# Optimization experiments

Hardware: AMD Instinct MI355X
Metric: run time of the kernel (lower is better)

Reference implementation:

```python
import jax, jax.numpy as jnp
import numpy as np

NUM_HEADS = 16
NUM_KV_HEADS = 4
HEAD_DIM = 128
ROPE_THETA = 10000.0


def _rope_cos_sin(T, dim, theta):
    inv_freq = 1.0 / (theta ** (jnp.arange(0, dim, 2, dtype=jnp.float32) / dim))
    freqs = jnp.arange(T, dtype=jnp.float32)[:, None] * inv_freq[None, :]  # (T, dim/2)
    emb = jnp.concatenate([freqs, freqs], axis=-1)  # (T, dim)
    return jnp.cos(emb), jnp.sin(emb)


def _rotate_half(x):
    h = x.shape[-1] // 2
    return jnp.concatenate([-x[..., h:], x[..., :h]], axis=-1)


def _apply_rope(x, cos, sin):
    # x: (B, H, T, D); cos/sin: (T, D)
    return x * cos[None, None] + _rotate_half(x) * sin[None, None]


def setup_inputs() -> dict:
    key = jax.random.key(0)
    ks = jax.random.split(key, 6)
    B, T, H = 2, 2048, 2048
    latent = 256
    kv_dim = NUM_KV_HEADS * HEAD_DIM
    s = 0.02
    return {
        "x": jax.random.normal(ks[0], (B, T, H), jnp.float32),
        "wq": jax.random.normal(ks[1], (H, H), jnp.float32) * s,
        "wkv": jax.random.normal(ks[2], (latent, H), jnp.float32) * s,
        "wk": jax.random.normal(ks[3], (kv_dim, latent), jnp.float32) * s,
        "wv": jax.random.normal(ks[4], (kv_dim, latent), jnp.float32) * s,
        "wo": jax.random.normal(ks[5], (H, H), jnp.float32) * s,
    }


def reference(x, wq, wkv, wk, wv, wo):
    B, T, hidden = x.shape
    nh, nkv, hd = NUM_HEADS, NUM_KV_HEADS, HEAD_DIM

    q = jnp.einsum('bth,dh->btd', x, wq)
    kv_latent = jnp.einsum('bth,lh->btl', x, wkv)
    k = jnp.einsum('btl,dl->btd', kv_latent, wk)
    v = jnp.einsum('btl,dl->btd', kv_latent, wv)

    q = q.reshape(B, T, nh, hd).transpose(0, 2, 1, 3)   # (B, nh, T, hd)
    k = k.reshape(B, T, nkv, hd).transpose(0, 2, 1, 3)  # (B, nkv, T, hd)
    v = v.reshape(B, T, nkv, hd).transpose(0, 2, 1, 3)

    cos, sin = _rope_cos_sin(T, hd, ROPE_THETA)
    q = _apply_rope(q, cos, sin)
    k = _apply_rope(k, cos, sin)

    rep = nh // nkv
    k = jnp.repeat(k, rep, axis=1)  # (B, nh, T, hd)
    v = jnp.repeat(v, rep, axis=1)

    scores = jnp.einsum('bhqd,bhkd->bhqk', q, k) * (1.0 / np.sqrt(hd))
    causal = jnp.triu(jnp.ones((T, T), dtype=bool), k=1)
    scores = jnp.where(causal[None, None], -jnp.inf, scores)
    probs = jax.nn.softmax(scores, axis=-1)
    out = jnp.einsum('bhqk,bhkd->bhqd', probs, v)
    out = out.transpose(0, 2, 1, 3).reshape(B, T, nh * hd)
    return jnp.einsum('btd,hd->bth', out, wo)
```

## Files before the change

kernel.cpp:

```cpp
#include <hip/hip_runtime.h>
#include <math.h>


#define AS1 __attribute__((address_space(1)))
#define AS3 __attribute__((address_space(3)))
#define QSTRIDE 2304

typedef short bf16x8 __attribute__((ext_vector_type(8)));
typedef float f32x4 __attribute__((ext_vector_type(4)));
typedef float f32x16 __attribute__((ext_vector_type(16)));
typedef unsigned int uint32x2 __attribute__((ext_vector_type(2)));

__device__ __forceinline__ unsigned short f2bf(float x) {
  union { float f; unsigned int u; } q; q.f = x;
  unsigned int u = q.u;
  u += 0x7FFFu + ((u >> 16) & 1u);
  return (unsigned short)(u >> 16);
}
__device__ __forceinline__ float bf2f(unsigned short x) {
  union { unsigned int u; float f; } q; q.u = ((unsigned int)x) << 16;
  return q.f;
}
__device__ __forceinline__ unsigned int pack2bf(float a, float b) {
  return (unsigned int)f2bf(a) | ((unsigned int)f2bf(b) << 16);
}
__device__ __forceinline__ uint32x2 plswap(unsigned int a, unsigned int b) {
  return __builtin_amdgcn_permlane32_swap(a, b, false, false);
}
__device__ __forceinline__ float xor32_add(float x) {
  union { float f; unsigned int u; } X; X.f = x;
  uint32x2 r = plswap(X.u, X.u);
  union { unsigned int u; float f; } A, B; A.u = r.x; B.u = r.y;
  return A.f + B.f;
}

__global__ __launch_bounds__(256) void rope_table(float* __restrict__ cost,
                                                  float* __restrict__ sint,
                                                  int T) {
  int idx = blockIdx.x * 256 + threadIdx.x;
  if (idx >= T * 64) return;
  int t = idx >> 6, j = idx & 63;
  double invf = pow(10000.0, -(double)j / 64.0);
  double ang = (double)t * invf;
  cost[idx] = (float)cos(ang);
  sint[idx] = (float)sin(ang);
}

__global__ __launch_bounds__(256) void conv_bf16(const float* __restrict__ src,
                                                 unsigned short* __restrict__ dst,
                                                 int n) {
  int i = (blockIdx.x * 256 + threadIdx.x) * 4;
  if (i >= n) return;
  float4 f = *(const float4*)(src + i);
  ushort4 o;
  o.x = f2bf(f.x); o.y = f2bf(f.y); o.z = f2bf(f.z); o.w = f2bf(f.w);
  *(ushort4*)(dst + i) = o;
}

template <bool OUT_BF16>
__global__ __launch_bounds__(256) void gemm_mfma(const unsigned short* __restrict__ A,
                                                 const unsigned short* __restrict__ W,
                                                 void* __restrict__ Cv,
                                                 int M, int N, int K,
                                                 int lda, int ldw, int ldc) {
  __shared__ unsigned short Asl[2][128 * 32];
  __shared__ unsigned short Wsl[2][128 * 32];
  int tid = threadIdx.x;
  int w = tid >> 6, lane = tid & 63;
  int g = lane >> 4, c = lane & 15;
  int wm = w >> 1, wn = w & 1;
  int m0 = blockIdx.y * 128, n0 = blockIdx.x * 128;

  f32x4 acc[4][4] = {};

#pragma unroll
  for (int i = 0; i < 2; ++i) {
    int idx = i * 256 + tid;
    int row = idx >> 2;
    int kk = (idx & 3) * 8;
    __builtin_amdgcn_global_load_lds(
        (const AS1 void*)(A + (size_t)(m0 + row) * lda + kk),
        (AS3 void*)(Asl[0] + ((size_t)i * 256 + (w << 6)) * 8), 16, 0, 0);
    __builtin_amdgcn_global_load_lds(
        (const AS1 void*)(W + (size_t)(n0 + row) * ldw + kk),
        (AS3 void*)(Wsl[0] + ((size_t)i * 256 + (w << 6)) * 8), 16, 0, 0);
  }
  __syncthreads();

  int cur = 0;
  for (int k0 = 0; k0 < K; k0 += 32) {
    if (k0 + 32 < K) {
      int nb = cur ^ 1;
#pragma unroll
      for (int i = 0; i < 2; ++i) {
        int idx = i * 256 + tid;
        int row = idx >> 2;
        int kk = (idx & 3) * 8;
        __builtin_amdgcn_global_load_lds(
            (const AS1 void*)(A + (size_t)(m0 + row) * lda + k0 + 32 + kk),
            (AS3 void*)(Asl[nb] + ((size_t)i * 256 + (w << 6)) * 8), 16, 0, 0);
        __builtin_amdgcn_global_load_lds(
            (const AS1 void*)(W + (size_t)(n0 + row) * ldw + k0 + 32 + kk),
            (AS3 void*)(Wsl[nb] + ((size_t)i * 256 + (w << 6)) * 8), 16, 0, 0);
      }
    }
    bf16x8 af[4], wf[4];
#pragma unroll
    for (int mi = 0; mi < 4; ++mi)
      af[mi] = *(const bf16x8*)(Asl[cur] + (wm * 64 + mi * 16 + c) * 32 + g * 8);
#pragma unroll
    for (int ni = 0; ni < 4; ++ni)
      wf[ni] = *(const bf16x8*)(Wsl[cur] + (wn * 64 + ni * 16 + c) * 32 + g * 8);
#pragma unroll
    for (int mi = 0; mi < 4; ++mi)
#pragma unroll
      for (int ni = 0; ni < 4; ++ni)
        acc[mi][ni] = __builtin_amdgcn_mfma_f32_16x16x32_bf16(af[mi], wf[ni],
                                                              acc[mi][ni], 0, 0, 0);
    __syncthreads();
    cur ^= 1;
  }
#pragma unroll
  for (int mi = 0; mi < 4; ++mi)
#pragma unroll
    for (int r = 0; r < 4; ++r) {
      size_t mrow = (size_t)(m0 + wm * 64 + mi * 16 + g * 4 + r) * ldc;
#pragma unroll
      for (int ni = 0; ni < 4; ++ni) {
        int n = n0 + wn * 64 + ni * 16 + c;
        if (OUT_BF16)
          ((unsigned short*)Cv)[mrow + n] = f2bf(acc[mi][ni][r]);
        else
          ((float*)Cv)[mrow + n] = acc[mi][ni][r];
      }
    }
}

__global__ __launch_bounds__(256) void rope_ip_bf16(unsigned short* __restrict__ buf,
                                                    int nheads, int T, int rowstride,
                                                    const float* __restrict__ cost,
                                                    const float* __restrict__ sint,
                                                    float scale) {
  int idx = blockIdx.x * 256 + threadIdx.x;
  int d = idx & 63;
  int rest = idx >> 6;
  int h = rest % nheads;
  int bt = rest / nheads;
  int t = bt & (T - 1);
  unsigned short* p = buf + (size_t)bt * rowstride + h * 128;
  float cc = cost[t * 64 + d], ss = sint[t * 64 + d];
  float x0 = bf2f(p[d]), x1 = bf2f(p[d + 64]);
  p[d]      = f2bf((x0 * cc - x1 * ss) * scale);
  p[d + 64] = f2bf((x1 * cc + x0 * ss) * scale);
}

__global__ __launch_bounds__(256) void rope_pack_k(const unsigned short* __restrict__ kvcat,
                                                   unsigned short* __restrict__ kp,
                                                   const float* __restrict__ cost,
                                                   const float* __restrict__ sint) {
  int idx = blockIdx.x * 256 + threadIdx.x;
  int d = idx & 63;
  int rest = idx >> 6;
  int kvh = rest & 3;
  int bt = rest >> 2;
  int t = bt & 2047, b = bt >> 11;
  const unsigned short* src = kvcat + (size_t)bt * 1024 + kvh * 128;
  float cc = cost[t * 64 + d], ss = sint[t * 64 + d];
  float x0 = bf2f(src[d]), x1 = bf2f(src[d + 64]);
  unsigned short y0 = f2bf(x0 * cc - x1 * ss);
  unsigned short y1 = f2bf(x1 * cc + x0 * ss);
  int kr = t & 63;
  size_t base = (size_t)(b * 4 + kvh) * 262144 + (size_t)(t >> 6) * 8192;
  kp[base + ((kr * 128 + d)      ^ ((kr & 7) << 3))] = y0;
  kp[base + ((kr * 128 + d + 64) ^ ((kr & 7) << 3))] = y1;
}

__global__ __launch_bounds__(256) void transpose_v(const unsigned short* __restrict__ kvcat,
                                                   unsigned short* __restrict__ vp) {
  __shared__ unsigned short tile[32][33];
  int t0 = blockIdx.x * 32, d0 = blockIdx.y * 32, b = blockIdx.z;
  int tx = threadIdx.x & 31, ty = threadIdx.x >> 5;
#pragma unroll
  for (int i = 0; i < 4; ++i) {
    int t = ty + i * 8;
    tile[t][tx] = kvcat[((size_t)(b * 2048 + t0 + t)) * 1024 + 512 + d0 + tx];
  }
  __syncthreads();
#pragma unroll
  for (int i = 0; i < 4; ++i) {
    int dd = ty + i * 8;
    int D = d0 + dd;
    int d = D & 127;
    int t = t0 + tx;
    size_t base = (size_t)(b * 4 + (D >> 7)) * 262144 + (size_t)(t >> 6) * 8192;
    vp[base + ((d * 64 + (t & 63)) ^ ((d & 7) << 3))] = tile[tx][dd];
  }
}

__global__ __launch_bounds__(256, 2) void attn_mfma(const unsigned short* __restrict__ qb,
                                                    const unsigned short* __restrict__ kp,
                                                    const unsigned short* __restrict__ vp,
                                                    unsigned short* __restrict__ attob) {
  __shared__ unsigned short kimg[2][8192];
  __shared__ unsigned short vimg[2][8192];

  int tid = threadIdx.x;
  int w = tid >> 6, lane = tid & 63;
  int cl = lane & 31, hi = lane >> 5;
  int stream = blockIdx.x & 31;
  int gseq = blockIdx.x >> 5;
  int g = (gseq & 1) ? (15 - (gseq >> 1)) : (gseq >> 1);
  int h = stream & 15, b = stream >> 4;
  int kvh = h >> 2;
  int q0w = g * 128 + w * 32;
  int nt = 2 * g + 2;

  const unsigned short* kpS = kp + (size_t)(b * 4 + kvh) * 262144;
  const unsigned short* vpS = vp + (size_t)(b * 4 + kvh) * 262144;

  bf16x8 qa[8];
  {
    const unsigned short* qrow = qb + ((size_t)(b * 2048 + q0w + cl)) * QSTRIDE + h * 128 + hi * 8;
#pragma unroll
    for (int kc = 0; kc < 8; ++kc)
      qa[kc] = *(const bf16x8*)(qrow + kc * 16);
  }

  f32x16 o0 = {}, o1 = {}, o2 = {}, o3 = {};
  float l = 0.f;

#pragma unroll
  for (int i = 0; i < 4; ++i) {
    __builtin_amdgcn_global_load_lds(
        (const AS1 void*)(kpS + (size_t)w * 2048 + i * 512 + lane * 8),
        (AS3 void*)(&kimg[0][w * 2048 + i * 512]), 16, 0, 0);
    __builtin_amdgcn_global_load_lds(
        (const AS1 void*)(vpS + (size_t)w * 2048 + i * 512 + lane * 8),
        (AS3 void*)(&vimg[0][w * 2048 + i * 512]), 16, 0, 0);
  }
  __syncthreads();

  int cur = 0;
  for (int ti = 0; ti < nt; ++ti) {
    if (ti + 1 < nt) {
      size_t src = (size_t)(ti + 1) * 8192 + w * 2048 + lane * 8;
      int nb = cur ^ 1;
#pragma unroll
      for (int i = 0; i < 4; ++i) {
        __builtin_amdgcn_global_load_lds(
            (const AS1 void*)(kpS + src + i * 512),
            (AS3 void*)(&kimg[nb][w * 2048 + i * 512]), 16, 0, 0);
        __builtin_amdgcn_global_load_lds(
            (const AS1 void*)(vpS + src + i * 512),
            (AS3 void*)(&vimg[nb][w * 2048 + i * 512]), 16, 0, 0);
      }
    }
#pragma unroll
    for (int s = 0; s < 2; ++s) {
      int ks0 = ti * 64 + s * 32;
      if (ks0 > q0w) continue;
      bf16x8 kf[8];
#pragma unroll
      for (int kc = 0; kc < 8; ++kc)
        kf[kc] = *(const bf16x8*)&kimg[cur][((s * 32 + cl) * 128 + kc * 16 + hi * 8)
                                            ^ ((cl & 7) << 3)];
      f32x16 sS = {};
      __builtin_amdgcn_s_setprio(1);
#pragma unroll
      for (int kc = 0; kc < 8; ++kc)
        sS = __builtin_amdgcn_mfma_f32_32x32x16_bf16(kf[kc], qa[kc], sS, 0, 0, 0);
      __builtin_amdgcn_s_setprio(0);
      bf16x8 vf[8];
#pragma unroll
      for (int db = 0; db < 4; ++db)
#pragma unroll
        for (int ks = 0; ks < 2; ++ks)
          vf[db * 2 + ks] = *(const bf16x8*)&vimg[cur][((db * 32 + cl) * 64
                              + s * 32 + ks * 16 + hi * 8) ^ ((cl & 7) << 3)];
      if (ks0 == q0w) {
#pragma unroll
        for (int r = 0; r < 16; ++r) {
          int krow = (r & 3) + 8 * (r >> 2) + 4 * hi;
          if (krow > cl) sS[r] = -INFINITY;
        }
      }
      float p[16];
      float rs = 0.f;
#pragma unroll
      for (int r = 0; r < 16; ++r) { p[r] = __expf(sS[r]); rs += p[r]; }
      l += rs;
      union { unsigned int u[4]; bf16x8 v; } pb0, pb1;
      {
        uint32x2 r0 = plswap(pack2bf(p[0], p[1]), pack2bf(p[4], p[5]));
        uint32x2 r1 = plswap(pack2bf(p[2], p[3]), pack2bf(p[6], p[7]));
        pb0.u[0] = r0.x; pb0.u[1] = r1.x; pb0.u[2] = r0.y; pb0.u[3] = r1.y;
        uint32x2 r2 = plswap(pack2bf(p[8], p[9]), pack2bf(p[12], p[13]));
        uint32x2 r3 = plswap(pack2bf(p[10], p[11]), pack2bf(p[14], p[15]));
        pb1.u[0] = r2.x; pb1.u[1] = r3.x; pb1.u[2] = r2.y; pb1.u[3] = r3.y;
      }
      __builtin_amdgcn_s_setprio(1);
      o0 = __builtin_amdgcn_mfma_f32_32x32x16_bf16(vf[0], pb0.v, o0, 0, 0, 0);
      o1 = __builtin_amdgcn_mfma_f32_32x32x16_bf16(vf[2], pb0.v, o1, 0, 0, 0);
      o2 = __builtin_amdgcn_mfma_f32_32x32x16_bf16(vf[4], pb0.v, o2, 0, 0, 0);
      o3 = __builtin_amdgcn_mfma_f32_32x32x16_bf16(vf[6], pb0.v, o3, 0, 0, 0);
      o0 = __builtin_amdgcn_mfma_f32_32x32x16_bf16(vf[1], pb1.v, o0, 0, 0, 0);
      o1 = __builtin_amdgcn_mfma_f32_32x32x16_bf16(vf[3], pb1.v, o1, 0, 0, 0);
      o2 = __builtin_amdgcn_mfma_f32_32x32x16_bf16(vf[5], pb1.v, o2, 0, 0, 0);
      o3 = __builtin_amdgcn_mfma_f32_32x32x16_bf16(vf[7], pb1.v, o3, 0, 0, 0);
      __builtin_amdgcn_s_setprio(0);
    }
    __syncthreads();
    cur ^= 1;
  }

  float lsum = xor32_add(l);
  float inv = 1.f / lsum;
  int q = q0w + cl;
  unsigned short* obase = attob + ((size_t)(b * 2048 + q)) * 2048 + h * 128;
#pragma unroll
  for (int r = 0; r < 16; ++r) {
    int dl = (r & 3) + 8 * (r >> 2) + 4 * hi;
    obase[dl]      = f2bf(o0[r] * inv);
    obase[32 + dl] = f2bf(o1[r] * inv);
    obase[64 + dl] = f2bf(o2[r] * inv);
    obase[96 + dl] = f2bf(o3[r] * inv);
  }
}

extern "C" void kernel_launch(void* const* d_in, const int* in_sizes, int n_in,
                              void* d_out, int out_size, void* d_ws, size_t ws_size,
                              hipStream_t stream) {
  const float* x   = (const float*)d_in[0];
  const float* wq  = (const float*)d_in[1];
  const float* wkv = (const float*)d_in[2];
  const float* wk  = (const float*)d_in[3];
  const float* wv  = (const float*)d_in[4];
  const float* wo  = (const float*)d_in[5];
  float* out = (float*)d_out;
  float* ws  = (float*)d_ws;

  const int B = 2, T = 2048, H = 2048, NH = 16, NKV = 4, LAT = 256, KVD = 512;
  const int BT = B * T;

  size_t off = 0;
  unsigned short* xb    = (unsigned short*)(ws + off); off += (size_t)BT * H / 2;
  unsigned short* wqb   = (unsigned short*)(ws + off); off += (size_t)H * H / 2;
  unsigned short* wkvb  = (unsigned short*)(ws + off); off += (size_t)LAT * H / 2;
  unsigned short* wkb   = (unsigned short*)(ws + off); off += (size_t)KVD * LAT / 2;
  unsigned short* wvb   = (unsigned short*)(ws + off); off += (size_t)KVD * LAT / 2;
  unsigned short* wob   = (unsigned short*)(ws + off); off += (size_t)H * H / 2;
  unsigned short* qkv   = (unsigned short*)(ws + off); off += (size_t)BT * QSTRIDE / 2;
  unsigned short* kvcat = (unsigned short*)(ws + off); off += (size_t)BT * 1024 / 2;
  unsigned short* kp    = (unsigned short*)(ws + off); off += (size_t)BT * KVD / 2;
  unsigned short* vp    = (unsigned short*)(ws + off); off += (size_t)BT * KVD / 2;
  unsigned short* attob = (unsigned short*)(ws + off); off += (size_t)BT * H / 2;
  float* cost = ws + off; off += (size_t)T * 64;
  float* sint = ws + off; off += (size_t)T * 64;

  const float scale = 0.088388347648318447f;

  rope_table<<<(T * 64 + 255) / 256, 256, 0, stream>>>(cost, sint, T);

  conv_bf16<<<(BT * H / 4) / 256, 256, 0, stream>>>(x, xb, BT * H);
  conv_bf16<<<(H * H / 4) / 256, 256, 0, stream>>>(wq, wqb, H * H);
  conv_bf16<<<(LAT * H / 4) / 256, 256, 0, stream>>>(wkv, wkvb, LAT * H);
  conv_bf16<<<(KVD * LAT / 4) / 256, 256, 0, stream>>>(wk, wkb, KVD * LAT);
  conv_bf16<<<(KVD * LAT / 4) / 256, 256, 0, stream>>>(wv, wvb, KVD * LAT);
  conv_bf16<<<(H * H / 4) / 256, 256, 0, stream>>>(wo, wob, H * H);

  gemm_mfma<true><<<dim3(QSTRIDE / 128, BT / 128), 256, 0, stream>>>(
      xb, wqb, qkv, BT, QSTRIDE, H, H, H, QSTRIDE);
  gemm_mfma<true><<<dim3(1024 / 128, BT / 128), 256, 0, stream>>>(
      qkv + H, wkb, kvcat, BT, 1024, LAT, QSTRIDE, LAT, 1024);

  rope_ip_bf16<<<(BT * NH * 64) / 256, 256, 0, stream>>>(qkv, NH, T, QSTRIDE, cost, sint, scale);
  rope_pack_k<<<(BT * NKV * 64) / 256, 256, 0, stream>>>(kvcat, kp, cost, sint);
  transpose_v<<<dim3(T / 32, KVD / 32, B), 256, 0, stream>>>(kvcat, vp);

  attn_mfma<<<512, 256, 0, stream>>>(qkv, kp, vp, attob);

  gemm_mfma<false><<<dim3(H / 128, BT / 128), 256, 0, stream>>>(
      attob, wob, out, BT, H, H, H, H, H);
}
```

Before: 231.8 us.

## Split attention KV tiles across waves with shared-memory reduction and smaller blocks

The attention kernel now uses 64-query blocks instead of 128, launches twice as many blocks, and uses 32-key tiles instead of 64-key tiles. Pairs of waves split the key tiles between them (even/odd) and combine their partial outputs and row sums through shared memory at the end. The K/V packing kernels change to a 32-row tile layout to match. LDS use per block drops, so the launch bound rises to 4 blocks per SM. This is meant to improve occupancy and load balance on the causal triangle. In exchange it adds a final reduction, rounds the partial outputs to bf16 before summing, and doubles the tile iterations per block.

```diff
diff --git a/kernel.cpp b/kernel.cpp
--- a/kernel.cpp
+++ b/kernel.cpp
@@ -169,8 +169,8 @@
   float x0 = bf2f(src[d]), x1 = bf2f(src[d + 64]);
   unsigned short y0 = f2bf(x0 * cc - x1 * ss);
   unsigned short y1 = f2bf(x1 * cc + x0 * ss);
-  int kr = t & 63;
-  size_t base = (size_t)(b * 4 + kvh) * 262144 + (size_t)(t >> 6) * 8192;
+  int kr = t & 31;
+  size_t base = (size_t)(b * 4 + kvh) * 262144 + (size_t)(t >> 5) * 4096;
   kp[base + ((kr * 128 + d)      ^ ((kr & 7) << 3))] = y0;
   kp[base + ((kr * 128 + d + 64) ^ ((kr & 7) << 3))] = y1;
 }
@@ -192,28 +192,27 @@
     int D = d0 + dd;
     int d = D & 127;
     int t = t0 + tx;
-    size_t base = (size_t)(b * 4 + (D >> 7)) * 262144 + (size_t)(t >> 6) * 8192;
-    vp[base + ((d * 64 + (t & 63)) ^ ((d & 7) << 3))] = tile[tx][dd];
-  }
-}
-
-__global__ __launch_bounds__(256, 2) void attn_mfma(const unsigned short* __restrict__ qb,
+    size_t base = (size_t)(b * 4 + (D >> 7)) * 262144 + (size_t)(t >> 5) * 4096;
+    vp[base + ((d * 32 + (t & 31)) ^ ((d & 3) << 3))] = tile[tx][dd];
+  }
+}
+
+__global__ __launch_bounds__(256, 4) void attn_mfma(const unsigned short* __restrict__ qb,
                                                     const unsigned short* __restrict__ kp,
                                                     const unsigned short* __restrict__ vp,
                                                     unsigned short* __restrict__ attob) {
-  __shared__ unsigned short kimg[2][8192];
-  __shared__ unsigned short vimg[2][8192];
+  __shared__ unsigned short smem[16896];
 
   int tid = threadIdx.x;
   int w = tid >> 6, lane = tid & 63;
+  int wq = w >> 1, wk = w & 1;
   int cl = lane & 31, hi = lane >> 5;
   int stream = blockIdx.x & 31;
-  int gseq = blockIdx.x >> 5;
-  int g = (gseq & 1) ? (15 - (gseq >> 1)) : (gseq >> 1);
+  int G = 31 - (blockIdx.x >> 5);
   int h = stream & 15, b = stream >> 4;
   int kvh = h >> 2;
-  int q0w = g * 128 + w * 32;
-  int nt = 2 * g + 2;
+  int q0w = G * 64 + wq * 32;
+  int nt = 2 * G + 2;
 
   const unsigned short* kpS = kp + (size_t)(b * 4 + kvh) * 262144;
   const unsigned short* vpS = vp + (size_t)(b * 4 + kvh) * 262144;
@@ -230,40 +229,39 @@
   float l = 0.f;
 
 #pragma unroll
-  for (int i = 0; i < 4; ++i) {
+  for (int i = 0; i < 2; ++i) {
     __builtin_amdgcn_global_load_lds(
-        (const AS1 void*)(kpS + (size_t)w * 2048 + i * 512 + lane * 8),
-        (AS3 void*)(&kimg[0][w * 2048 + i * 512]), 16, 0, 0);
+        (const AS1 void*)(kpS + (size_t)w * 1024 + i * 512 + lane * 8),
+        (AS3 void*)(&smem[w * 1024 + i * 512]), 16, 0, 0);
     __builtin_amdgcn_global_load_lds(
-        (const AS1 void*)(vpS + (size_t)w * 2048 + i * 512 + lane * 8),
-        (AS3 void*)(&vimg[0][w * 2048 + i * 512]), 16, 0, 0);
+        (const AS1 void*)(vpS + (size_t)w * 1024 + i * 512 + lane * 8),
+        (AS3 void*)(&smem[8192 + w * 1024 + i * 512]), 16, 0, 0);
   }
   __syncthreads();
 
   int cur = 0;
   for (int ti = 0; ti < nt; ++ti) {
     if (ti + 1 < nt) {
-      size_t src = (size_t)(ti + 1) * 8192 + w * 2048 + lane * 8;
+      size_t src = (size_t)(ti + 1) * 4096 + w * 1024 + lane * 8;
       int nb = cur ^ 1;
 #pragma unroll
-      for (int i = 0; i < 4; ++i) {
+      for (int i = 0; i < 2; ++i) {
         __builtin_amdgcn_global_load_lds(
             (const AS1 void*)(kpS + src + i * 512),
-            (AS3 void*)(&kimg[nb][w * 2048 + i * 512]), 16, 0, 0);
+            (AS3 void*)(&smem[nb * 4096 + w * 1024 + i * 512]), 16, 0, 0);
         __builtin_amdgcn_global_load_lds(
             (const AS1 void*)(vpS + src + i * 512),
-            (AS3 void*)(&vimg[nb][w * 2048 + i * 512]), 16, 0, 0);
+            (AS3 void*)(&smem[8192 + nb * 4096 + w * 1024 + i * 512]), 16, 0, 0);
       }
     }
-#pragma unroll
-    for (int s = 0; s < 2; ++s) {
-      int ks0 = ti * 64 + s * 32;
-      if (ks0 > q0w) continue;
+    int ks0 = ti << 5;
+    if (((ti & 1) == wk) && (ks0 <= q0w)) {
+      const unsigned short* kb_ = &smem[cur * 4096];
+      const unsigned short* vb_ = &smem[8192 + cur * 4096];
       bf16x8 kf[8];
 #pragma unroll
       for (int kc = 0; kc < 8; ++kc)
-        kf[kc] = *(const bf16x8*)&kimg[cur][((s * 32 + cl) * 128 + kc * 16 + hi * 8)
-                                            ^ ((cl & 7) << 3)];
+        kf[kc] = *(const bf16x8*)&kb_[(cl * 128 + kc * 16 + hi * 8) ^ ((cl & 7) << 3)];
       f32x16 sS = {};
       __builtin_amdgcn_s_setprio(1);
 #pragma unroll
@@ -275,8 +273,8 @@
       for (int db = 0; db < 4; ++db)
 #pragma unroll
         for (int ks = 0; ks < 2; ++ks)
-          vf[db * 2 + ks] = *(const bf16x8*)&vimg[cur][((db * 32 + cl) * 64
-                              + s * 32 + ks * 16 + hi * 8) ^ ((cl & 7) << 3)];
+          vf[db * 2 + ks] = *(const bf16x8*)&vb_[((db * 32 + cl) * 32
+                              + ks * 16 + hi * 8) ^ ((cl & 3) << 3)];
       if (ks0 == q0w) {
 #pragma unroll
         for (int r = 0; r < 16; ++r) {
@@ -314,16 +312,37 @@
   }
 
   float lsum = xor32_add(l);
-  float inv = 1.f / lsum;
-  int q = q0w + cl;
-  unsigned short* obase = attob + ((size_t)(b * 2048 + q)) * 2048 + h * 128;
+  float* lptr = (float*)&smem[16384];
+  int qr = wq * 32 + cl;
+  if (hi == 0) lptr[wk * 64 + qr] = lsum;
 #pragma unroll
   for (int r = 0; r < 16; ++r) {
     int dl = (r & 3) + 8 * (r >> 2) + 4 * hi;
-    obase[dl]      = f2bf(o0[r] * inv);
-    obase[32 + dl] = f2bf(o1[r] * inv);
-    obase[64 + dl] = f2bf(o2[r] * inv);
-    obase[96 + dl] = f2bf(o3[r] * inv);
+    smem[wk * 8192 + qr * 128 + dl]      = f2bf(o0[r]);
+    smem[wk * 8192 + qr * 128 + 32 + dl] = f2bf(o1[r]);
+    smem[wk * 8192 + qr * 128 + 64 + dl] = f2bf(o2[r]);
+    smem[wk * 8192 + qr * 128 + 96 + dl] = f2bf(o3[r]);
+  }
+  __syncthreads();
+
+  {
+    int q = tid >> 2;
+    int dc = (tid & 3) * 32;
+    float inv = 1.f / (lptr[q] + lptr[64 + q]);
+    unsigned short* orow = attob + ((size_t)(b * 2048 + G * 64 + q)) * 2048 + h * 128 + dc;
+#pragma unroll
+    for (int i4 = 0; i4 < 4; ++i4) {
+      bf16x8 a = *(const bf16x8*)&smem[q * 128 + dc + i4 * 8];
+      bf16x8 c = *(const bf16x8*)&smem[8192 + q * 128 + dc + i4 * 8];
+      union { unsigned int u[4]; bf16x8 v; } ov;
+#pragma unroll
+      for (int j = 0; j < 4; ++j) {
+        float s0 = (bf2f((unsigned short)a[j * 2])     + bf2f((unsigned short)c[j * 2]))     * inv;
+        float s1 = (bf2f((unsigned short)a[j * 2 + 1]) + bf2f((unsigned short)c[j * 2 + 1])) * inv;
+        ov.u[j] = pack2bf(s0, s1);
+      }
+      *(bf16x8*)(orow + i4 * 8) = ov.v;
+    }
   }
 }
 
@@ -377,7 +396,7 @@
   rope_pack_k<<<(BT * NKV * 64) / 256, 256, 0, stream>>>(kvcat, kp, cost, sint);
   transpose_v<<<dim3(T / 32, KVD / 32, B), 256, 0, stream>>>(kvcat, vp);
 
-  attn_mfma<<<512, 256, 0, stream>>>(qkv, kp, vp, attob);
+  attn_mfma<<<1024, 256, 0, stream>>>(qkv, kp, vp, attob);
 
   gemm_mfma<false><<<dim3(H / 128, BT / 128), 256, 0, stream>>>(
       attob, wob, out, BT, H, H, H, H, H);
```

Result: slower. 407.3 us (+75.7%).
